# Kernel tuning notes

Measured on AMD Instinct MI355X. Metric: run time of the kernel, lower is better.

## Reference

```python
import jax, jax.numpy as jnp
import numpy as np

N, E, H = 4096, 256, 8
DH = E // H
BS = 8
EPS = 1e-5


def setup_inputs() -> dict:
    key = jax.random.key(0)
    ks = jax.random.split(key, 12)
    xav = lambda k, shape: jax.random.uniform(k, shape, jnp.float32,
                                              -np.sqrt(6.0 / (shape[0] + shape[1])),
                                              np.sqrt(6.0 / (shape[0] + shape[1])))
    return {
        "x": jax.random.normal(ks[0], (N, E), jnp.float32),
        "pe": jax.random.normal(ks[1], (N, E), jnp.float32),
        "x_batch": jnp.sort(jax.random.randint(ks[2], (N,), 0, BS)).astype(jnp.int64),
        "Wq": xav(ks[3], (E, E)),
        "Wk": xav(ks[4], (E, E)),
        "Wv": xav(ks[5], (E, E)),
        "bq": jnp.zeros((E,), jnp.float32),
        "bk": jnp.zeros((E,), jnp.float32),
        "bv": jnp.zeros((E,), jnp.float32),
        "Wo": xav(ks[6], (E, E)),
        "bo": jnp.zeros((E,), jnp.float32),
        "gamma": jnp.ones((E,), jnp.float32),
        "beta": jnp.zeros((E,), jnp.float32),
    }


def reference(x, pe, x_batch, Wq, Wk, Wv, bq, bk, bv, Wo, bo, gamma, beta):
    # per-batch self-attention == global attention with block-diagonal mask
    xp = x + pe                                   # q and k get pos-embed, v does not
    q = (xp @ Wq.T + bq).reshape(N, H, DH)
    k = (xp @ Wk.T + bk).reshape(N, H, DH)
    v = (x @ Wv.T + bv).reshape(N, H, DH)
    scale = 1.0 / np.sqrt(DH)
    same = x_batch[:, None] == x_batch[None, :]   # [N, N] intra-batch mask
    scores = jnp.einsum('ihd,jhd->hij', q, k) * scale
    scores = jnp.where(same[None], scores, -jnp.inf)
    attn = jax.nn.softmax(scores, axis=-1)        # dropout=0 (eval)
    ctx = jnp.einsum('hij,jhd->ihd', attn, v).reshape(N, E)
    out = ctx @ Wo.T + bo
    y = out + x                                   # layer_drop=0; residual is v == x
    mu = jnp.mean(y, axis=-1, keepdims=True)
    var = jnp.mean((y - mu) ** 2, axis=-1, keepdims=True)
    return (y - mu) / jnp.sqrt(var + EPS) * gamma + beta
```

## Files before the change

kernel.cpp:

```cpp
#include <hip/hip_runtime.h>
#include <math.h>

namespace {

constexpr int N  = 4096;
constexpr int E  = 256;
constexpr int H  = 8;
constexpr int DH = 32;
constexpr int BS = 8;
constexpr float CL = 0.17677669529663687f * 1.4426950408889634f;

typedef __bf16 bf16x8 __attribute__((ext_vector_type(8)));
typedef __bf16 bf16x4 __attribute__((ext_vector_type(4)));
typedef float  f32x4  __attribute__((ext_vector_type(4)));

#if __has_builtin(__builtin_amdgcn_exp2f)
#define EXP2F(x) __builtin_amdgcn_exp2f(x)
#else
#define EXP2F(x) __expf((x) * 0.6931471805599453f)
#endif

__device__ inline bf16x8 pack8(float4 a, float4 b) {
  bf16x8 r;
  r[0] = (__bf16)a.x; r[1] = (__bf16)a.y; r[2] = (__bf16)a.z; r[3] = (__bf16)a.w;
  r[4] = (__bf16)b.x; r[5] = (__bf16)b.y; r[6] = (__bf16)b.z; r[7] = (__bf16)b.w;
  return r;
}


__global__ __launch_bounds__(256) void prep_kernel(
    const float* __restrict__ x, const float* __restrict__ pe,
    const int* __restrict__ xb,
    const float* __restrict__ Wq, const float* __restrict__ Wk,
    const float* __restrict__ Wv, const float* __restrict__ Wo,
    __bf16* __restrict__ xpef, __bf16* __restrict__ xvf,
    __bf16* __restrict__ wfrag, int* __restrict__ seg)
{
  const int bid  = blockIdx.x;
  const int wv4  = threadIdx.x >> 6;
  const int lane = threadIdx.x & 63;
  const int l15  = lane & 15, g = lane >> 4;

  if (bid < 512) {
    const int wid = bid * 4 + wv4;
    const int rt = wid >> 3, kt = wid & 7;
    const float* xr = x  + (size_t)(rt * 16 + l15) * E + kt * 32 + 8 * g;
    const float* pr = pe + (size_t)(rt * 16 + l15) * E + kt * 32 + 8 * g;
    float4 a0 = *(const float4*)xr;
    float4 a1 = *(const float4*)(xr + 4);
    const float4 p0 = *(const float4*)pr;
    const float4 p1 = *(const float4*)(pr + 4);
    *reinterpret_cast<bf16x8*>(xvf + (size_t)wid * 512 + lane * 8) = pack8(a0, a1);
    a0.x += p0.x; a0.y += p0.y; a0.z += p0.z; a0.w += p0.w;
    a1.x += p1.x; a1.y += p1.y; a1.z += p1.z; a1.w += p1.w;
    *reinterpret_cast<bf16x8*>(xpef + (size_t)wid * 512 + lane * 8) = pack8(a0, a1);
  } else if (bid < 640) {
    const int wid = (bid - 512) * 4 + wv4;
    const int mat = wid >> 7;
    const int rem = wid & 127;
    const int n16 = rem >> 3, kt = rem & 7;
    const float* __restrict__ W =
        (mat == 0) ? Wq : (mat == 1) ? Wk : (mat == 2) ? Wv : Wo;
    const float* wr = W + (size_t)(n16 * 16 + l15) * E + kt * 32 + 8 * g;
    *reinterpret_cast<bf16x8*>(wfrag + (size_t)wid * 512 + lane * 8) =
        pack8(*(const float4*)wr, *(const float4*)(wr + 4));
  } else {
    if (threadIdx.x <= BS) {
      const int t = threadIdx.x;
      int lo = 0, hi = N;
      while (lo < hi) { int mid = (lo + hi) >> 1; if (xb[mid] < t) lo = mid + 1; else hi = mid; }
      seg[t] = lo;
    }
  }
}

__global__ __launch_bounds__(256) void qkv_mfma(
    const __bf16* __restrict__ xpef, const __bf16* __restrict__ xvf,
    const __bf16* __restrict__ wfrag,
    const float* __restrict__ bq, const float* __restrict__ bk,
    const float* __restrict__ bv,
    __bf16* __restrict__ qfrag, __bf16* __restrict__ kfrag,
    __bf16* __restrict__ vfrag)
{
  const int mat  = blockIdx.y;
  const int rt   = blockIdx.x;
  const int wv   = threadIdx.x >> 6;
  const int lane = threadIdx.x & 63;
  const int l15  = lane & 15, g = lane >> 4;
  const int m0   = rt * 16;

  const __bf16* __restrict__ A = (mat < 2) ? xpef : xvf;
  const __bf16* __restrict__ W = wfrag + (size_t)mat * 65536;

  bf16x8 af[8];
#pragma unroll
  for (int kk = 0; kk < 8; ++kk)
    af[kk] = *reinterpret_cast<const bf16x8*>(A + (size_t)(rt * 8 + kk) * 512 + lane * 8);

  const int token = m0 + l15;

#pragma unroll
  for (int p = 0; p < 2; ++p) {
    const int cb0  = wv * 64 + p * 32;
    const int n16b = cb0 >> 4;
    const __bf16* __restrict__ Wp0 = W + (size_t)(n16b * 8) * 512 + lane * 8;
    const __bf16* __restrict__ Wp1 = W + (size_t)((n16b + 1) * 8) * 512 + lane * 8;

    f32x4 acc0 = {0.f, 0.f, 0.f, 0.f};
    f32x4 acc1 = {0.f, 0.f, 0.f, 0.f};

    bf16x8 ww[4];
    ww[0] = *reinterpret_cast<const bf16x8*>(Wp0);
    ww[1] = *reinterpret_cast<const bf16x8*>(Wp1);
    ww[2] = *reinterpret_cast<const bf16x8*>(Wp0 + 512);
    ww[3] = *reinterpret_cast<const bf16x8*>(Wp1 + 512);

#pragma unroll
    for (int kk = 0; kk < 8; ++kk) {
      const bf16x8 cw0 = ww[(2 * kk) & 3];
      const bf16x8 cw1 = ww[(2 * kk + 1) & 3];
      if (kk < 6) {
        ww[(2 * kk) & 3]     = *reinterpret_cast<const bf16x8*>(Wp0 + (size_t)(kk + 2) * 512);
        ww[(2 * kk + 1) & 3] = *reinterpret_cast<const bf16x8*>(Wp1 + (size_t)(kk + 2) * 512);
      }
      acc0 = __builtin_amdgcn_mfma_f32_16x16x32_bf16(cw0, af[kk], acc0, 0, 0, 0);
      acc1 = __builtin_amdgcn_mfma_f32_16x16x32_bf16(cw1, af[kk], acc1, 0, 0, 0);
    }

    const f32x4 accs[2] = {acc0, acc1};
    if (mat < 2) {
      const float* __restrict__ bi = mat ? bk : bq;
      __bf16* __restrict__ dst = mat ? kfrag : qfrag;
#pragma unroll
      for (int nt = 0; nt < 2; ++nt) {
        const int e  = cb0 + nt * 16 + 4 * g;
        const float4 bb = *(const float4*)(bi + e);
        const int h  = e >> 5;
        const int gp = (e & 31) >> 3;
        const int ib = e & 7;
        bf16x4 o;
        o.x = (__bf16)(accs[nt][0] + bb.x);
        o.y = (__bf16)(accs[nt][1] + bb.y);
        o.z = (__bf16)(accs[nt][2] + bb.z);
        o.w = (__bf16)(accs[nt][3] + bb.w);
        size_t idx;
        if (mat == 0) {
          const int lp = (token & 15) + 16 * gp;
          idx = ((size_t)(h * 256 + rt) * 64 + lp) * 8 + ib;
        } else {
          const int t  = token >> 6, tk = token & 63;
          const int mt = 2 * (tk >> 5) + ((tk >> 2) & 1);
          const int lp = 4 * ((tk >> 3) & 3) + (tk & 3) + 16 * gp;
          idx = ((size_t)((h * 64 + t) * 4 + mt) * 64 + lp) * 8 + ib;
        }
        *reinterpret_cast<bf16x4*>(dst + idx) = o;
      }
    } else {
      const int t  = token >> 6, tk = token & 63;
      const int ks = (tk >> 5) & 1;
      const int gp = (tk >> 3) & 3;
      const int i  = tk & 7;
#pragma unroll
      for (int nt = 0; nt < 2; ++nt) {
        const int e0 = cb0 + nt * 16 + 4 * g;
        const float4 bb = *(const float4*)(bv + e0);
        const float bbr[4] = {bb.x, bb.y, bb.z, bb.w};
#pragma unroll
        for (int r = 0; r < 4; ++r) {
          const int d  = e0 + r;
          const int h  = d >> 5, dh = (d >> 4) & 1;
          const size_t idx =
              ((size_t)(((h * 64 + t) * 2 + ks) * 2 + dh) * 64 + (d & 15) + 16 * gp) * 8 + i;
          vfrag[idx] = (__bf16)(accs[nt][r] + bbr[r]);
        }
      }
    }
  }
}

__global__ __launch_bounds__(512) void attn_proj_ln(
    const __bf16* __restrict__ qfrag, const __bf16* __restrict__ kfrag,
    const __bf16* __restrict__ vfrag, const int* __restrict__ xb,
    const int* __restrict__ seg,
    const float* __restrict__ x, const __bf16* __restrict__ wofrag,
    const float* __restrict__ bo, const float* __restrict__ gamma,
    const float* __restrict__ beta, float* __restrict__ out)
{
  const int rt   = blockIdx.x;
  const int m0   = rt * 16;
  const int h    = threadIdx.x >> 6;
  const int lane = threadIdx.x & 63;
  const int l15  = lane & 15;
  const int g    = lane >> 4;
  const int qrow = m0 + l15;

  __shared__ __bf16 cl[16][264];
  __shared__ float redS[8][16];
  __shared__ float redQ[8][16];

  bf16x8 wreg[2][8];
#pragma unroll
  for (int nt = 0; nt < 2; ++nt)
#pragma unroll
    for (int kk = 0; kk < 8; ++kk)
      wreg[nt][kk] = *reinterpret_cast<const bf16x8*>(
          wofrag + (size_t)((h * 2 + nt) * 8 + kk) * 512 + lane * 8);

  {
    const int b  = xb[qrow];
    const int lo = seg[b];
    const int hi = seg[b + 1];

    const bf16x8 qf = *reinterpret_cast<const bf16x8*>(
        qfrag + (size_t)(h * 256 + rt) * 512 + lane * 8);

    const int kstart = __shfl(lo, 0, 64);
    const int kend   = __shfl(hi, 15, 64);

    f32x4 acc0 = {0.f, 0.f, 0.f, 0.f};
    f32x4 acc1 = {0.f, 0.f, 0.f, 0.f};
    float lsum = 0.f;

    for (int t = kstart >> 6; t * 64 < kend; ++t) {
      const int j0 = t * 64;
      const __bf16* kb4 = kfrag + (size_t)(h * 64 + t) * 2048 + lane * 8;
      const __bf16* vb4 = vfrag + (size_t)(h * 64 + t) * 2048 + lane * 8;

      const bf16x8 kf0 = *reinterpret_cast<const bf16x8*>(kb4);
      const bf16x8 kf1 = *reinterpret_cast<const bf16x8*>(kb4 + 512);
      const bf16x8 kf2 = *reinterpret_cast<const bf16x8*>(kb4 + 1024);
      const bf16x8 kf3 = *reinterpret_cast<const bf16x8*>(kb4 + 1536);
      const bf16x8 vf00 = *reinterpret_cast<const bf16x8*>(vb4);
      const bf16x8 vf01 = *reinterpret_cast<const bf16x8*>(vb4 + 512);
      const bf16x8 vf10 = *reinterpret_cast<const bf16x8*>(vb4 + 1024);
      const bf16x8 vf11 = *reinterpret_cast<const bf16x8*>(vb4 + 1536);

      const f32x4 z = {0.f, 0.f, 0.f, 0.f};
      f32x4 s[4];
      s[0] = __builtin_amdgcn_mfma_f32_16x16x32_bf16(kf0, qf, z, 0, 0, 0);
      s[1] = __builtin_amdgcn_mfma_f32_16x16x32_bf16(kf1, qf, z, 0, 0, 0);
      s[2] = __builtin_amdgcn_mfma_f32_16x16x32_bf16(kf2, qf, z, 0, 0, 0);
      s[3] = __builtin_amdgcn_mfma_f32_16x16x32_bf16(kf3, qf, z, 0, 0, 0);

      bf16x8 pa[2];
#pragma unroll
      for (int ks = 0; ks < 2; ++ks)
#pragma unroll
        for (int b_ = 0; b_ < 2; ++b_)
#pragma unroll
          for (int r = 0; r < 4; ++r) {
            const int key = j0 + 32 * ks + 8 * g + 4 * b_ + r;
            const float sc = s[2 * ks + b_][r] * CL;
            const float e  = (key >= lo && key < hi) ? EXP2F(sc) : 0.f;
            lsum += e;
            pa[ks][4 * b_ + r] = (__bf16)e;
          }

      acc0 = __builtin_amdgcn_mfma_f32_16x16x32_bf16(pa[0], vf00, acc0, 0, 0, 0);
      acc1 = __builtin_amdgcn_mfma_f32_16x16x32_bf16(pa[0], vf01, acc1, 0, 0, 0);
      acc0 = __builtin_amdgcn_mfma_f32_16x16x32_bf16(pa[1], vf10, acc0, 0, 0, 0);
      acc1 = __builtin_amdgcn_mfma_f32_16x16x32_bf16(pa[1], vf11, acc1, 0, 0, 0);
    }

    lsum += __shfl_xor(lsum, 16, 64);
    lsum += __shfl_xor(lsum, 32, 64);
    const float inv = 1.0f / lsum;
    float invr[4];
#pragma unroll
    for (int r = 0; r < 4; ++r) invr[r] = __shfl(inv, 4 * g + r, 64);

#pragma unroll
    for (int r = 0; r < 4; ++r) {
      cl[4 * g + r][h * DH + l15]      = (__bf16)(acc0[r] * invr[r]);
      cl[4 * g + r][h * DH + 16 + l15] = (__bf16)(acc1[r] * invr[r]);
    }
  }
  __syncthreads();

  {
    bf16x8 af[8];
#pragma unroll
    for (int kk = 0; kk < 8; ++kk)
      af[kk] = *reinterpret_cast<const bf16x8*>(&cl[l15][kk * 32 + 8 * g]);

    f32x4 acc[2];
    acc[0] = f32x4{0.f, 0.f, 0.f, 0.f};
    acc[1] = f32x4{0.f, 0.f, 0.f, 0.f};

#pragma unroll
    for (int kk = 0; kk < 8; ++kk)
#pragma unroll
      for (int nt = 0; nt < 2; ++nt)
        acc[nt] = __builtin_amdgcn_mfma_f32_16x16x32_bf16(af[kk], wreg[nt][kk],
                                                          acc[nt], 0, 0, 0);

    float yv[2][4];
    float s1[4], s2[4];
#pragma unroll
    for (int r = 0; r < 4; ++r) { s1[r] = 0.f; s2[r] = 0.f; }
#pragma unroll
    for (int nt = 0; nt < 2; ++nt) {
      const int c = h * 32 + nt * 16 + l15;
      const float bb = bo[c];
#pragma unroll
      for (int r = 0; r < 4; ++r) {
        const int row = m0 + 4 * g + r;
        const float y = acc[nt][r] + bb + x[(size_t)row * E + c];
        yv[nt][r] = y;
        s1[r] += y;
        s2[r] += y * y;
      }
    }
#pragma unroll
    for (int off = 1; off < 16; off <<= 1) {
#pragma unroll
      for (int r = 0; r < 4; ++r) {
        s1[r] += __shfl_xor(s1[r], off, 64);
        s2[r] += __shfl_xor(s2[r], off, 64);
      }
    }
    if (l15 == 0) {
#pragma unroll
      for (int r = 0; r < 4; ++r) {
        redS[h][4 * g + r] = s1[r];
        redQ[h][4 * g + r] = s2[r];
      }
    }
    __syncthreads();
    float mu[4], rs[4];
#pragma unroll
    for (int r = 0; r < 4; ++r) {
      float ts = 0.f, tq = 0.f;
#pragma unroll
      for (int w = 0; w < 8; ++w) { ts += redS[w][4 * g + r]; tq += redQ[w][4 * g + r]; }
      mu[r] = ts * (1.0f / E);
      const float var = tq * (1.0f / E) - mu[r] * mu[r];
      rs[r] = rsqrtf(var + 1e-5f);
    }
#pragma unroll
    for (int nt = 0; nt < 2; ++nt) {
      const int c = h * 32 + nt * 16 + l15;
      const float gg = gamma[c];
      const float bt = beta[c];
#pragma unroll
      for (int r = 0; r < 4; ++r) {
        const int row = m0 + 4 * g + r;
        out[(size_t)row * E + c] = (yv[nt][r] - mu[r]) * rs[r] * gg + bt;
      }
    }
  }
}

}

extern "C" void kernel_launch(void* const* d_in, const int* in_sizes, int n_in,
                              void* d_out, int out_size, void* d_ws, size_t ws_size,
                              hipStream_t stream) {
  const float* x     = (const float*)d_in[0];
  const float* pe    = (const float*)d_in[1];
  const int*   xb    = (const int*)d_in[2];
  const float* Wq    = (const float*)d_in[3];
  const float* Wk    = (const float*)d_in[4];
  const float* Wv    = (const float*)d_in[5];
  const float* bq    = (const float*)d_in[6];
  const float* bk    = (const float*)d_in[7];
  const float* bv    = (const float*)d_in[8];
  const float* Wo    = (const float*)d_in[9];
  const float* bo    = (const float*)d_in[10];
  const float* gamma = (const float*)d_in[11];
  const float* beta  = (const float*)d_in[12];
  float* out = (float*)d_out;

  __bf16* ws = (__bf16*)d_ws;
  const size_t NE = (size_t)N * E;
  __bf16* qfrag = ws;
  __bf16* kfrag = ws + NE;
  __bf16* vfrag = ws + 2 * NE;
  __bf16* xpef  = ws + 3 * NE;
  __bf16* xvf   = ws + 4 * NE;
  __bf16* wfrag = ws + 5 * NE;
  int*    seg   = (int*)(ws + 5 * NE + 4 * 65536);

  prep_kernel<<<dim3(641), 256, 0, stream>>>(x, pe, xb, Wq, Wk, Wv, Wo,
                                             xpef, xvf, wfrag, seg);
  qkv_mfma<<<dim3(256, 3), 256, 0, stream>>>(xpef, xvf, wfrag, bq, bk, bv,
                                             qfrag, kfrag, vfrag);
  attn_proj_ln<<<dim3(256), 512, 0, stream>>>(qfrag, kfrag, vfrag, xb, seg,
                                              x, wfrag + 3 * 65536,
                                              bo, gamma, beta, out);
}
```

Before: 38.82 us.

## Split attention key loop across two waves per head and merge partials

Doubles the attention block to 1024 threads so each head gets two waves that process alternating 64-key tiles, then merges the unnormalized partial contexts and softmax sums through shared memory before the output projection. The output projection and LayerNorm are re-split so each of the 16 waves computes one 16-column tile. The goal is to halve the serial key-loop latency per block, since only 256 blocks run on a large GPU. The cost is an extra bf16 rounding of partial accumulators, more shared memory and register pressure under the larger launch bound.

```diff
diff --git a/kernel.cpp b/kernel.cpp
--- a/kernel.cpp
+++ b/kernel.cpp
@@ -178,7 +178,7 @@
   }
 }
 
-__global__ __launch_bounds__(512) void attn_proj_ln(
+__global__ __launch_bounds__(1024) void attn_proj_ln(
     const __bf16* __restrict__ qfrag, const __bf16* __restrict__ kfrag,
     const __bf16* __restrict__ vfrag, const int* __restrict__ xb,
     const int* __restrict__ seg,
@@ -188,23 +188,24 @@
 {
   const int rt   = blockIdx.x;
   const int m0   = rt * 16;
-  const int h    = threadIdx.x >> 6;
+  const int wv   = threadIdx.x >> 6;
+  const int h    = wv & 7;
+  const int s    = wv >> 3;
   const int lane = threadIdx.x & 63;
   const int l15  = lane & 15;
   const int g    = lane >> 4;
   const int qrow = m0 + l15;
 
-  __shared__ __bf16 cl[16][264];
-  __shared__ float redS[8][16];
-  __shared__ float redQ[8][16];
-
-  bf16x8 wreg[2][8];
-#pragma unroll
-  for (int nt = 0; nt < 2; ++nt)
-#pragma unroll
-    for (int kk = 0; kk < 8; ++kk)
-      wreg[nt][kk] = *reinterpret_cast<const bf16x8*>(
-          wofrag + (size_t)((h * 2 + nt) * 8 + kk) * 512 + lane * 8);
+  __shared__ __bf16 cl[2][16][264];
+  __shared__ float  lsW[2][8][16];
+  __shared__ float  redS[16][16];
+  __shared__ float  redQ[16][16];
+
+  bf16x8 wreg[8];
+#pragma unroll
+  for (int kk = 0; kk < 8; ++kk)
+    wreg[kk] = *reinterpret_cast<const bf16x8*>(
+        wofrag + (size_t)(wv * 8 + kk) * 512 + lane * 8);
 
   {
     const int b  = xb[qrow];
@@ -216,12 +217,13 @@
 
     const int kstart = __shfl(lo, 0, 64);
     const int kend   = __shfl(hi, 15, 64);
+    const int t0     = kstart >> 6;
 
     f32x4 acc0 = {0.f, 0.f, 0.f, 0.f};
     f32x4 acc1 = {0.f, 0.f, 0.f, 0.f};
     float lsum = 0.f;
 
-    for (int t = kstart >> 6; t * 64 < kend; ++t) {
+    for (int t = t0 + s; t * 64 < kend; t += 2) {
       const int j0 = t * 64;
       const __bf16* kb4 = kfrag + (size_t)(h * 64 + t) * 2048 + lane * 8;
       const __bf16* vb4 = vfrag + (size_t)(h * 64 + t) * 2048 + lane * 8;
@@ -236,11 +238,11 @@
       const bf16x8 vf11 = *reinterpret_cast<const bf16x8*>(vb4 + 1536);
 
       const f32x4 z = {0.f, 0.f, 0.f, 0.f};
-      f32x4 s[4];
-      s[0] = __builtin_amdgcn_mfma_f32_16x16x32_bf16(kf0, qf, z, 0, 0, 0);
-      s[1] = __builtin_amdgcn_mfma_f32_16x16x32_bf16(kf1, qf, z, 0, 0, 0);
-      s[2] = __builtin_amdgcn_mfma_f32_16x16x32_bf16(kf2, qf, z, 0, 0, 0);
-      s[3] = __builtin_amdgcn_mfma_f32_16x16x32_bf16(kf3, qf, z, 0, 0, 0);
+      f32x4 sc4[4];
+      sc4[0] = __builtin_amdgcn_mfma_f32_16x16x32_bf16(kf0, qf, z, 0, 0, 0);
+      sc4[1] = __builtin_amdgcn_mfma_f32_16x16x32_bf16(kf1, qf, z, 0, 0, 0);
+      sc4[2] = __builtin_amdgcn_mfma_f32_16x16x32_bf16(kf2, qf, z, 0, 0, 0);
+      sc4[3] = __builtin_amdgcn_mfma_f32_16x16x32_bf16(kf3, qf, z, 0, 0, 0);
 
       bf16x8 pa[2];
 #pragma unroll
@@ -250,7 +252,7 @@
 #pragma unroll
           for (int r = 0; r < 4; ++r) {
             const int key = j0 + 32 * ks + 8 * g + 4 * b_ + r;
-            const float sc = s[2 * ks + b_][r] * CL;
+            const float sc = sc4[2 * ks + b_][r] * CL;
             const float e  = (key >= lo && key < hi) ? EXP2F(sc) : 0.f;
             lsum += e;
             pa[ks][4 * b_ + r] = (__bf16)e;
@@ -264,15 +266,12 @@
 
     lsum += __shfl_xor(lsum, 16, 64);
     lsum += __shfl_xor(lsum, 32, 64);
-    const float inv = 1.0f / lsum;
-    float invr[4];
-#pragma unroll
-    for (int r = 0; r < 4; ++r) invr[r] = __shfl(inv, 4 * g + r, 64);
+    if (lane < 16) lsW[s][h][lane] = lsum;
 
 #pragma unroll
     for (int r = 0; r < 4; ++r) {
-      cl[4 * g + r][h * DH + l15]      = (__bf16)(acc0[r] * invr[r]);
-      cl[4 * g + r][h * DH + 16 + l15] = (__bf16)(acc1[r] * invr[r]);
+      cl[s][4 * g + r][h * DH + l15]      = (__bf16)(acc0[r]);
+      cl[s][4 * g + r][h * DH + 16 + l15] = (__bf16)(acc1[r]);
     }
   }
   __syncthreads();
@@ -280,36 +279,31 @@
   {
     bf16x8 af[8];
 #pragma unroll
+    for (int kk = 0; kk < 8; ++kk) {
+      const int cc = kk * 32 + 8 * g;
+      const bf16x8 a0 = *reinterpret_cast<const bf16x8*>(&cl[0][l15][cc]);
+      const bf16x8 a1 = *reinterpret_cast<const bf16x8*>(&cl[1][l15][cc]);
+      const float inv = 1.0f / (lsW[0][kk][l15] + lsW[1][kk][l15]);
+#pragma unroll
+      for (int i = 0; i < 8; ++i)
+        af[kk][i] = (__bf16)(((float)a0[i] + (float)a1[i]) * inv);
+    }
+
+    f32x4 acc = {0.f, 0.f, 0.f, 0.f};
+#pragma unroll
     for (int kk = 0; kk < 8; ++kk)
-      af[kk] = *reinterpret_cast<const bf16x8*>(&cl[l15][kk * 32 + 8 * g]);
-
-    f32x4 acc[2];
-    acc[0] = f32x4{0.f, 0.f, 0.f, 0.f};
-    acc[1] = f32x4{0.f, 0.f, 0.f, 0.f};
-
-#pragma unroll
-    for (int kk = 0; kk < 8; ++kk)
-#pragma unroll
-      for (int nt = 0; nt < 2; ++nt)
-        acc[nt] = __builtin_amdgcn_mfma_f32_16x16x32_bf16(af[kk], wreg[nt][kk],
-                                                          acc[nt], 0, 0, 0);
-
-    float yv[2][4];
-    float s1[4], s2[4];
-#pragma unroll
-    for (int r = 0; r < 4; ++r) { s1[r] = 0.f; s2[r] = 0.f; }
-#pragma unroll
-    for (int nt = 0; nt < 2; ++nt) {
-      const int c = h * 32 + nt * 16 + l15;
-      const float bb = bo[c];
-#pragma unroll
-      for (int r = 0; r < 4; ++r) {
-        const int row = m0 + 4 * g + r;
-        const float y = acc[nt][r] + bb + x[(size_t)row * E + c];
-        yv[nt][r] = y;
-        s1[r] += y;
-        s2[r] += y * y;
-      }
+      acc = __builtin_amdgcn_mfma_f32_16x16x32_bf16(af[kk], wreg[kk], acc, 0, 0, 0);
+
+    const int c = wv * 16 + l15;
+    const float bb = bo[c];
+    float yv[4], s1[4], s2[4];
+#pragma unroll
+    for (int r = 0; r < 4; ++r) {
+      const int row = m0 + 4 * g + r;
+      const float y = acc[r] + bb + x[(size_t)row * E + c];
+      yv[r] = y;
+      s1[r] = y;
+      s2[r] = y * y;
     }
 #pragma unroll
     for (int off = 1; off < 16; off <<= 1) {
@@ -322,8 +316,8 @@
     if (l15 == 0) {
 #pragma unroll
       for (int r = 0; r < 4; ++r) {
-        redS[h][4 * g + r] = s1[r];
-        redQ[h][4 * g + r] = s2[r];
+        redS[wv][4 * g + r] = s1[r];
+        redQ[wv][4 * g + r] = s2[r];
       }
     }
     __syncthreads();
@@ -332,21 +326,20 @@
     for (int r = 0; r < 4; ++r) {
       float ts = 0.f, tq = 0.f;
 #pragma unroll
-      for (int w = 0; w < 8; ++w) { ts += redS[w][4 * g + r]; tq += redQ[w][4 * g + r]; }
+      for (int w = 0; w < 16; ++w) {
+        ts += redS[w][4 * g + r];
+        tq += redQ[w][4 * g + r];
+      }
       mu[r] = ts * (1.0f / E);
       const float var = tq * (1.0f / E) - mu[r] * mu[r];
       rs[r] = rsqrtf(var + 1e-5f);
     }
-#pragma unroll
-    for (int nt = 0; nt < 2; ++nt) {
-      const int c = h * 32 + nt * 16 + l15;
-      const float gg = gamma[c];
-      const float bt = beta[c];
-#pragma unroll
-      for (int r = 0; r < 4; ++r) {
-        const int row = m0 + 4 * g + r;
-        out[(size_t)row * E + c] = (yv[nt][r] - mu[r]) * rs[r] * gg + bt;
-      }
+    const float gg = gamma[c];
+    const float bt = beta[c];
+#pragma unroll
+    for (int r = 0; r < 4; ++r) {
+      const int row = m0 + 4 * g + r;
+      out[(size_t)row * E + c] = (yv[r] - mu[r]) * rs[r] * gg + bt;
     }
   }
 }
@@ -385,7 +378,7 @@
                                              xpef, xvf, wfrag, seg);
   qkv_mfma<<<dim3(256, 3), 256, 0, stream>>>(xpef, xvf, wfrag, bq, bk, bv,
                                              qfrag, kfrag, vfrag);
-  attn_proj_ln<<<dim3(256), 512, 0, stream>>>(qfrag, kfrag, vfrag, xb, seg,
-                                              x, wfrag + 3 * 65536,
-                                              bo, gamma, beta, out);
-}
+  attn_proj_ln<<<dim3(256), 1024, 0, stream>>>(qfrag, kfrag, vfrag, xb, seg,
+                                               x, wfrag + 3 * 65536,
+                                               bo, gamma, beta, out);
+}
```

After: 41.63 us. 7.2% more time.
